# Kernel optimization log

Hardware: AMD Instinct MI355X
Metric: run time of the kernel (lower is better)

## Reference

```python
import jax, jax.numpy as jnp
import numpy as np
import math

B, T, C = 2, 2048, 2048
H, G, HS = 16, 4, 128  # n_head, n_query_groups, head_size
EPS = 1e-5
SCALE = 1.0 / math.sqrt(HS)
QKV_DIM = (H + 2 * G) * HS  # 3072, gate logits (H) appended after


def _build_rope(seq_len, n_elem, base):
    freq = base ** (np.arange(0, n_elem, 2, dtype=np.float64) / n_elem)
    inv_freq = 1.0 / freq
    idx_theta = np.outer(np.arange(seq_len, dtype=np.float64), inv_freq)
    return (jnp.asarray(np.cos(idx_theta), dtype=jnp.float32),
            jnp.asarray(np.sin(idx_theta), dtype=jnp.float32))


def setup_inputs() -> dict:
    key = jax.random.key(0)
    k1, k2, k3 = jax.random.split(key, 3)
    x = jax.random.normal(k1, (B, T, C), dtype=jnp.float32)
    # rope base per module: 0.09 * local_window ** 1.628
    base = 0.09 * (2048.0 ** 1.628)
    cos, sin = _build_rope(T, HS, base)  # [T, HS//2]
    W_attn = jax.random.normal(k2, (QKV_DIM + H, C), dtype=jnp.float32) * 0.02
    W_proj = jax.random.normal(k3, (C, H * HS), dtype=jnp.float32) * 0.02
    q_norm_w = jnp.ones((HS,), dtype=jnp.float32)
    k_norm_w = jnp.ones((HS,), dtype=jnp.float32)
    return {"x": x, "cos": cos, "sin": sin, "W_attn": W_attn,
            "q_norm_w": q_norm_w, "k_norm_w": k_norm_w, "W_proj": W_proj}


def _rms_norm(v, w):
    # per-head RMSNorm over last dim (head_size)
    ms = jnp.mean(jnp.square(v), axis=-1, keepdims=True)
    return v * jax.lax.rsqrt(ms + EPS) * w


def _apply_rope(v, cos, sin):
    # v: [B, T, N, HS]; cos/sin: [T, HS//2]; non-interleaved halves
    d2 = v.shape[-1] // 2
    x1, x2 = v[..., :d2], v[..., d2:]
    c = cos[None, :, None, :]
    s = sin[None, :, None, :]
    return jnp.concatenate([x1 * c - x2 * s, x2 * c + x1 * s], axis=-1)


def reference(x, cos, sin, W_attn, q_norm_w, k_norm_w, W_proj):
    qkv = jnp.einsum('btc,oc->bto', x, W_attn)  # [B, T, QKV_DIM+H]
    q = qkv[..., : H * HS].reshape(B, T, H, HS)
    k = qkv[..., H * HS:(H + G) * HS].reshape(B, T, G, HS)
    v = qkv[..., (H + G) * HS: QKV_DIM].reshape(B, T, G, HS)
    gate = qkv[..., QKV_DIM:]  # [B, T, H]

    q = _apply_rope(_rms_norm(q, q_norm_w), cos, sin)
    k = _apply_rope(_rms_norm(k, k_norm_w), cos, sin)

    rep = H // G
    kr = jnp.repeat(k, rep, axis=2)  # [B, T, H, HS]
    vr = jnp.repeat(v, rep, axis=2)

    scores = jnp.einsum('bthd,bshd->bhts', q, kr) * SCALE  # [B, H, T, T]
    causal = jnp.tril(jnp.ones((T, T), dtype=bool))
    scores = jnp.where(causal, scores, jnp.finfo(scores.dtype).min)
    probs = jax.nn.softmax(scores, axis=-1)
    out = jnp.einsum('bhts,bshd->bthd', probs, vr)  # [B, T, H, HS]

    out = out * jax.nn.sigmoid(gate)[..., None]  # gated attention, per-head
    y = jnp.einsum('bto,co->btc', out.reshape(B, T, H * HS), W_proj)
    return y
```

## Files before the change

kernel.cpp:

```cpp
#include <hip/hip_runtime.h>

#define T_   2048
#define BB   2
#define CC   2048
#define HH   16
#define GG   4
#define HSS  128
#define QKVD 3072
#define NQKV 3088
#define NPAD 3200
#define SCALE_ 0.08838834764831845f
#define SCALE2_ (0.08838834764831845f * 1.4426950408889634f)

typedef __attribute__((ext_vector_type(8))) short  short8;
typedef __attribute__((ext_vector_type(4))) float  f32x4;
typedef __attribute__((ext_vector_type(4))) int    v4i;
typedef __attribute__((ext_vector_type(4))) float  v4f;
typedef __attribute__((ext_vector_type(4))) unsigned short u16x4;

typedef const void __attribute__((address_space(1)))* gas1_t;
typedef void __attribute__((address_space(3)))* as3_t;

__device__ __forceinline__ void gl_lds16(const void* g, void* l) {
    __builtin_amdgcn_global_load_lds((gas1_t)g, (as3_t)l, 16, 0, 0);
}

__device__ __forceinline__ unsigned short f2bf(float f) {
    unsigned u = __float_as_uint(f);
    u += 0x7fffu + ((u >> 16) & 1u);
    return (unsigned short)(u >> 16);
}
__device__ __forceinline__ float bf2f(unsigned short h) {
    return __uint_as_float(((unsigned)h) << 16);
}

template <int CTRL>
__device__ __forceinline__ float dppmv(float x) {
    int i = __float_as_int(x);
    return __int_as_float(__builtin_amdgcn_update_dpp(i, i, CTRL, 0xF, 0xF, false));
}
__device__ __forceinline__ void red16_max(float* v) {
#pragma unroll
    for (int r = 0; r < 4; ++r) v[r] = fmaxf(v[r], dppmv<0xB1>(v[r]));
#pragma unroll
    for (int r = 0; r < 4; ++r) v[r] = fmaxf(v[r], dppmv<0x4E>(v[r]));
#pragma unroll
    for (int r = 0; r < 4; ++r) v[r] = fmaxf(v[r], dppmv<0x124>(v[r]));
#pragma unroll
    for (int r = 0; r < 4; ++r) v[r] = fmaxf(v[r], dppmv<0x128>(v[r]));
}
__device__ __forceinline__ void red16_sum(float* v) {
#pragma unroll
    for (int r = 0; r < 4; ++r) v[r] += dppmv<0xB1>(v[r]);
#pragma unroll
    for (int r = 0; r < 4; ++r) v[r] += dppmv<0x4E>(v[r]);
#pragma unroll
    for (int r = 0; r < 4; ++r) v[r] += dppmv<0x124>(v[r]);
#pragma unroll
    for (int r = 0; r < 4; ++r) v[r] += dppmv<0x128>(v[r]);
}

__global__ void k_convert3(const float* __restrict__ x, const float* __restrict__ wa,
                           const float* __restrict__ wp,
                           unsigned short* __restrict__ xb, unsigned short* __restrict__ wab,
                           unsigned short* __restrict__ wpb) {
    const int id = blockIdx.x;
    const float* src; unsigned short* dst; int base, n_src4;
    if (id < 8192)       { src = x;  dst = xb;  base = id;         n_src4 = 2097152; }
    else if (id < 14592) { src = wa; dst = wab; base = id - 8192;  n_src4 = 1581056; }
    else                 { src = wp; dst = wpb; base = id - 14592; n_src4 = 1048576; }
    int i = base * 256 + threadIdx.x;
    u16x4 o;
    if (i < n_src4) {
        v4f v = *(const v4f*)(src + (size_t)i * 4);
        o[0] = f2bf(v[0]); o[1] = f2bf(v[1]); o[2] = f2bf(v[2]); o[3] = f2bf(v[3]);
    } else {
        o[0] = 0; o[1] = 0; o[2] = 0; o[3] = 0;
    }
    *(u16x4*)(dst + (size_t)i * 4) = o;
}

template <int BM_, typename OutT>
__launch_bounds__(512, 2)
__global__ void k_gemm8(const unsigned short* __restrict__ A,
                        const unsigned short* __restrict__ Bm,
                        OutT* __restrict__ C,
                        int K, int lda, int ldb, int ldc, int nmax) {
    constexpr int MI  = BM_ / 32;
    constexpr int NPH = MI / 2;
    __shared__ unsigned short As[2][BM_ * 64];
    __shared__ unsigned short Bs[2][256 * 64];
    const int t = threadIdx.x;
    const int lane = t & 63;
    const int wid  = t >> 6;
    const int wr = wid >> 2, wc = wid & 3;
    const int bm = blockIdx.x, bn = blockIdx.y;
    const int fro = lane & 15, fk = lane >> 4;

    const int srow  = lane >> 3;
    const size_t scol = (size_t)(((lane & 7) ^ srow) * 8);

    const unsigned short* Abase = A  + (size_t)(bm * BM_) * lda;
    const unsigned short* Bbase = Bm + (size_t)(bn * 256) * ldb;

    f32x4 acc[MI][4];
#pragma unroll
    for (int i = 0; i < MI; ++i)
#pragma unroll
        for (int j = 0; j < 4; ++j) acc[i][j] = (f32x4){0.f, 0.f, 0.f, 0.f};

#pragma unroll
    for (int h = 0; h < 2; ++h)
#pragma unroll
        for (int c8 = 0; c8 < 2; ++c8) {
            const int rr = h * 128 + wid * 16 + c8 * 8;
            if (BM_ == 256 || h == 0)
                gl_lds16(Abase + (size_t)(rr + srow) * lda + scol, &As[0][rr * 64]);
            gl_lds16(Bbase + (size_t)(rr + srow) * ldb + scol, &Bs[0][rr * 64]);
        }

    int cur = 0;
    for (int kt = 0; kt < K; kt += 64) {
        asm volatile("s_waitcnt vmcnt(0)" ::: "memory");
        __builtin_amdgcn_s_barrier();
        __builtin_amdgcn_sched_barrier(0);
        const bool pf = (kt + 64 < K);
        const int nxt = cur ^ 1;
        const int kn = kt + 64;

        short8 bf_[4][2];
#pragma unroll
        for (int q = 0; q < NPH; ++q) {
            short8 af[2][2];
#pragma unroll
            for (int im = 0; im < 2; ++im)
#pragma unroll
                for (int kk = 0; kk < 2; ++kk) {
                    const int ar = wr * (BM_ / 2) + (q * 2 + im) * 16 + fro;
                    af[im][kk] = *(const short8*)&As[cur][ar * 64 + ((kk * 4 + fk) ^ (ar & 7)) * 8];
                }
            if (q == 0) {
#pragma unroll
                for (int ni = 0; ni < 4; ++ni)
#pragma unroll
                    for (int kk = 0; kk < 2; ++kk) {
                        const int br = wc * 64 + ni * 16 + fro;
                        bf_[ni][kk] = *(const short8*)&Bs[cur][br * 64 + ((kk * 4 + fk) ^ (br & 7)) * 8];
                    }
            }
            if (pf) {
                if (BM_ == 256) {
                    const int h = q & 1;
#pragma unroll
                    for (int c8 = 0; c8 < 2; ++c8) {
                        const int rr = h * 128 + wid * 16 + c8 * 8;
                        if ((q >> 1) == 0)
                            gl_lds16(Abase + (size_t)(rr + srow) * lda + kn + scol, &As[nxt][rr * 64]);
                        else
                            gl_lds16(Bbase + (size_t)(rr + srow) * ldb + kn + scol, &Bs[nxt][rr * 64]);
                    }
                } else {
                    if (q == 0) {
#pragma unroll
                        for (int c8 = 0; c8 < 2; ++c8) {
                            const int rr = wid * 16 + c8 * 8;
                            gl_lds16(Abase + (size_t)(rr + srow) * lda + kn + scol, &As[nxt][rr * 64]);
                        }
                    } else {
#pragma unroll
                        for (int h = 0; h < 2; ++h)
#pragma unroll
                            for (int c8 = 0; c8 < 2; ++c8) {
                                const int rr = h * 128 + wid * 16 + c8 * 8;
                                gl_lds16(Bbase + (size_t)(rr + srow) * ldb + kn + scol, &Bs[nxt][rr * 64]);
                            }
                    }
                }
            }
            __builtin_amdgcn_s_setprio(1);
#pragma unroll
            for (int im = 0; im < 2; ++im)
#pragma unroll
                for (int ni = 0; ni < 4; ++ni)
#pragma unroll
                    for (int kk = 0; kk < 2; ++kk)
                        acc[q * 2 + im][ni] = __builtin_amdgcn_mfma_f32_16x16x32_bf16(
                            af[im][kk], bf_[ni][kk], acc[q * 2 + im][ni], 0, 0, 0);
            __builtin_amdgcn_s_setprio(0);
            __builtin_amdgcn_s_barrier();
        }
        cur ^= 1;
    }

    const int col16 = lane & 15, rbase = (lane >> 4) * 4;
    const int gr0 = bm * BM_ + wr * (BM_ / 2);
    const int gc0 = bn * 256 + wc * 64;
#pragma unroll
    for (int mi = 0; mi < MI; ++mi)
#pragma unroll
        for (int ni = 0; ni < 4; ++ni) {
            const int gcol = gc0 + ni * 16 + col16;
            if (gcol < nmax) {
#pragma unroll
                for (int r = 0; r < 4; ++r) {
                    const int grow = gr0 + mi * 16 + rbase + r;
                    float v = acc[mi][ni][r];
                    if constexpr (sizeof(OutT) == 2)
                        C[(size_t)grow * ldc + gcol] = (OutT)f2bf(v);
                    else
                        C[(size_t)grow * ldc + gcol] = (OutT)v;
                }
            }
        }
}

__global__ void k_normtrans(unsigned short* __restrict__ qkv,
                            const float* __restrict__ cosT, const float* __restrict__ sinT,
                            const float* __restrict__ qw, const float* __restrict__ kw,
                            unsigned short* __restrict__ vt) {
    __shared__ unsigned short tile[64][65];
    const int id = blockIdx.x;
    if (id < 20480) {
        const int lane = threadIdx.x & 63;
        const int row  = id * 4 + (threadIdx.x >> 6);
        const int tok  = row / 20;
        const int hh   = row - tok * 20;
        const int tpos = tok & (T_ - 1);
        unsigned short* rp = qkv + (size_t)tok * NPAD + (hh < 16 ? hh * 128 : 2048 + (hh - 16) * 128);
        const float* w = (hh < 16) ? qw : kw;
        float e1 = bf2f(rp[lane]);
        float e2 = bf2f(rp[lane + 64]);
        float ss = e1 * e1 + e2 * e2;
#pragma unroll
        for (int m = 1; m < 64; m <<= 1) ss += __shfl_xor(ss, m);
        float inv = rsqrtf(ss * (1.0f / 128.0f) + 1e-5f);
        float n1 = e1 * inv * w[lane];
        float n2 = e2 * inv * w[lane + 64];
        float c = cosT[tpos * 64 + lane];
        float s = sinT[tpos * 64 + lane];
        rp[lane]      = f2bf(n1 * c - n2 * s);
        rp[lane + 64] = f2bf(n2 * c + n1 * s);
    } else {
        const int t2 = id - 20480;
        const int b = (t2 & 7) >> 2, g = t2 & 3;
        const int s0 = ((t2 >> 3) & 31) * 64, d0 = (t2 >> 8) * 64;
        const int tx = threadIdx.x & 63, ty0 = threadIdx.x >> 6;
        const unsigned short* src = qkv + (size_t)(b * T_ + s0) * NPAD + 2560 + g * 128 + d0;
#pragma unroll
        for (int r = 0; r < 16; ++r) {
            int ty = ty0 * 16 + r;
            tile[ty][tx] = src[(size_t)ty * NPAD + tx];
        }
        __syncthreads();
        unsigned short* dstp = vt + ((size_t)(b * GG + g) * 128 + d0) * T_ + s0;
#pragma unroll
        for (int r = 0; r < 16; ++r) {
            int ty = ty0 * 16 + r;
            dstp[(size_t)ty * T_ + tx] = tile[tx][ty];
        }
    }
}

__launch_bounds__(512, 4)
__global__ void k_attn(const unsigned short* __restrict__ qkv,
                       const unsigned short* __restrict__ vt,
                       unsigned short* __restrict__ ao) {
    __shared__ unsigned short Ks[2][64 * 128];
    __shared__ unsigned short Vs[2][128 * 64];
    __shared__ unsigned short Ps[8][16 * 64];
    const int t = threadIdx.x;
    const int lane = t & 63;
    const int wid  = t >> 6;
    const int id = blockIdx.x;
    const int bg = id & 7;
    const int hh = (id >> 3) & 3;
    const int prx = (id >> 5) & 7;
    const int pr = (id & 256) ? (15 - prx) : prx;
    const int b = bg >> 2, g = bg & 3, h = g * 4 + hh;
    const int fro = lane & 15, fk = lane >> 4;
    const int rbase = fk * 4;

    const int qt  = (wid < 4) ? pr : 31 - pr;
    const int wq  = wid & 3;
    const int q0w = qt * 64 + wq * 16;
    const int nt_own  = qt + 1;
    const int nt_loop = 32 - pr;

    const unsigned short* kg0 = qkv + (size_t)(b * T_) * NPAD + 2048 + g * 128;
    const unsigned short* vg0 = vt + (size_t)(b * GG + g) * 128 * T_;

    short8 qf[4];
    const unsigned short* qp = qkv + (size_t)(b * T_ + q0w + fro) * NPAD + h * 128 + fk * 8;
#pragma unroll
    for (int kb = 0; kb < 4; ++kb) qf[kb] = *(const short8*)(qp + kb * 32);

    float m_r[4], l_r[4];
    f32x4 o[8];
#pragma unroll
    for (int r = 0; r < 4; ++r) { m_r[r] = -1e30f; l_r[r] = 0.f; }
#pragma unroll
    for (int d = 0; d < 8; ++d) o[d] = (f32x4){0.f, 0.f, 0.f, 0.f};

    const int cp0 = wid * 2;
    int cur = 0;

#pragma unroll
    for (int p = 0; p < 2; ++p) {
        const int cp = cp0 + p;
        const int kr = cp * 4 + (lane >> 4);
        const int sK = lane & 15;
        gl_lds16(kg0 + (size_t)kr * NPAD + (size_t)((sK ^ (kr & 7)) * 8), &Ks[cur][cp * 512]);
        const int d  = cp * 8 + (lane >> 3);
        const int sV = lane & 7;
        gl_lds16(vg0 + (size_t)d * T_ + (size_t)((sV ^ (d & 7)) * 8), &Vs[cur][cp * 512]);
    }
    __syncthreads();

    for (int ti = 0; ti < nt_loop; ++ti) {
        if (ti + 1 < nt_loop) {
            const int sn = (ti + 1) * 64;
#pragma unroll
            for (int p = 0; p < 2; ++p) {
                const int cp = cp0 + p;
                const int kr = cp * 4 + (lane >> 4);
                const int sK = lane & 15;
                gl_lds16(kg0 + (size_t)(sn + kr) * NPAD + (size_t)((sK ^ (kr & 7)) * 8), &Ks[cur ^ 1][cp * 512]);
                const int d  = cp * 8 + (lane >> 3);
                const int sV = lane & 7;
                gl_lds16(vg0 + (size_t)d * T_ + sn + (size_t)((sV ^ (d & 7)) * 8), &Vs[cur ^ 1][cp * 512]);
            }
        }
        if (ti < nt_own) {
            f32x4 sc[4];
#pragma unroll
            for (int jb = 0; jb < 4; ++jb) sc[jb] = (f32x4){0.f, 0.f, 0.f, 0.f};
#pragma unroll
            for (int jb = 0; jb < 4; ++jb) {
                const int kr = jb * 16 + fro;
#pragma unroll
                for (int kb = 0; kb < 4; ++kb) {
                    short8 kf = *(const short8*)&Ks[cur][kr * 128 + 8 * ((kb * 4 + fk) ^ (kr & 7))];
                    sc[jb] = __builtin_amdgcn_mfma_f32_16x16x32_bf16(qf[kb], kf, sc[jb], 0, 0, 0);
                }
            }
            const bool domask = (ti == qt);
#pragma unroll
            for (int jb = 0; jb < 4; ++jb)
#pragma unroll
                for (int r = 0; r < 4; ++r) {
                    float v = sc[jb][r] * SCALE2_;
                    if (domask && (jb * 16 + fro) > (wq * 16 + rbase + r)) v = -1e30f;
                    sc[jb][r] = v;
                }
            float mx[4], rs[4];
#pragma unroll
            for (int r = 0; r < 4; ++r)
                mx[r] = fmaxf(fmaxf(sc[0][r], sc[1][r]), fmaxf(sc[2][r], sc[3][r]));
            red16_max(mx);
            bool grow = false;
#pragma unroll
            for (int r = 0; r < 4; ++r) grow = grow || (mx[r] > m_r[r] + 8.f);
            if (__any(grow ? 1 : 0)) {
#pragma unroll
                for (int r = 0; r < 4; ++r) {
                    float mn = fmaxf(m_r[r], mx[r]);
                    float fs = exp2f(m_r[r] - mn);
                    m_r[r] = mn;
                    l_r[r] *= fs;
#pragma unroll
                    for (int d = 0; d < 8; ++d) o[d][r] *= fs;
                }
            }
#pragma unroll
            for (int jb = 0; jb < 4; ++jb)
#pragma unroll
                for (int r = 0; r < 4; ++r) sc[jb][r] = exp2f(sc[jb][r] - m_r[r]);
#pragma unroll
            for (int r = 0; r < 4; ++r)
                rs[r] = (sc[0][r] + sc[1][r]) + (sc[2][r] + sc[3][r]);
            red16_sum(rs);
#pragma unroll
            for (int r = 0; r < 4; ++r) l_r[r] += rs[r];
            unsigned short* pw = &Ps[wid][0];
#pragma unroll
            for (int jb = 0; jb < 4; ++jb)
#pragma unroll
                for (int r = 0; r < 4; ++r) {
                    const int row = rbase + r;
                    const int slot = jb * 2 + (fro >> 3);
                    pw[row * 64 + ((slot ^ (row & 7)) * 8 + (fro & 7))] = f2bf(sc[jb][r]);
                }
            asm volatile("s_waitcnt lgkmcnt(0)" ::: "memory");
            __builtin_amdgcn_sched_barrier(0);
            short8 pa[2];
#pragma unroll
            for (int ks = 0; ks < 2; ++ks)
                pa[ks] = *(const short8*)&Ps[wid][fro * 64 + ((ks * 4 + fk) ^ (fro & 7)) * 8];
#pragma unroll
            for (int ks = 0; ks < 2; ++ks)
#pragma unroll
                for (int db = 0; db < 8; ++db) {
                    const int d = db * 16 + fro;
                    short8 vf = *(const short8*)&Vs[cur][d * 64 + 8 * ((ks * 4 + fk) ^ (d & 7))];
                    o[db] = __builtin_amdgcn_mfma_f32_16x16x32_bf16(pa[ks], vf, o[db], 0, 0, 0);
                }
        }
        __syncthreads();
        cur ^= 1;
    }
#pragma unroll
    for (int r = 0; r < 4; ++r) {
        const int qrow = q0w + rbase + r;
        float gv = bf2f(qkv[(size_t)(b * T_ + qrow) * NPAD + QKVD + h]);
        float sg = 1.f / (1.f + __expf(-gv));
        float invl = sg / l_r[r];
        unsigned short* orow = ao + (size_t)(b * T_ + qrow) * 2048 + h * 128;
#pragma unroll
        for (int db = 0; db < 8; ++db)
            orow[db * 16 + fro] = f2bf(o[db][r] * invl);
    }
}

extern "C" void kernel_launch(void* const* d_in, const int* in_sizes, int n_in,
                              void* d_out, int out_size, void* d_ws, size_t ws_size,
                              hipStream_t stream) {
    const float* x      = (const float*)d_in[0];
    const float* cosT   = (const float*)d_in[1];
    const float* sinT   = (const float*)d_in[2];
    const float* W_attn = (const float*)d_in[3];
    const float* qw     = (const float*)d_in[4];
    const float* kw     = (const float*)d_in[5];
    const float* W_proj = (const float*)d_in[6];

    char* ws = (char*)d_ws;
    const size_t OFF_XB   = 0;
    const size_t OFF_WAB  = 16777216;
    const size_t OFF_WPB  = 29884416;
    const size_t OFF_QKV  = 38273024;
    const size_t OFF_VT   = 64487424;
    const size_t OFF_AO   = 68681728;
    const size_t NEED     = 85458944;
    if (ws_size < NEED) return;

    unsigned short* xb   = (unsigned short*)(ws + OFF_XB);
    unsigned short* wab  = (unsigned short*)(ws + OFF_WAB);
    unsigned short* wpb  = (unsigned short*)(ws + OFF_WPB);
    unsigned short* qkvb = (unsigned short*)(ws + OFF_QKV);
    unsigned short* vtb  = (unsigned short*)(ws + OFF_VT);
    unsigned short* aob  = (unsigned short*)(ws + OFF_AO);

    k_convert3<<<18688, 256, 0, stream>>>(x, W_attn, W_proj, xb, wab, wpb);
    k_gemm8<256, unsigned short><<<dim3(16, 13), 512, 0, stream>>>(xb, wab, qkvb, 2048, 2048, 2048, NPAD, NPAD);
    k_normtrans<<<20992, 256, 0, stream>>>(qkvb, cosT, sinT, qw, kw, vtb);
    k_attn<<<512, 512, 0, stream>>>(qkvb, vtb, aob);
    k_gemm8<128, float><<<dim3(32, 8), 512, 0, stream>>>(aob, wpb, (float*)d_out, 2048, 2048, 2048, 2048, 2048);
}
```

Before: 212.0 us.

## Single-buffer K/V tiles for higher occupancy and fold softmax scale into Q

Drops the double-buffered K/V LDS tiles for a single buffer loaded synchronously each iteration, which halves LDS use so launch bounds can ask for 6 waves per SIMD instead of 4. The softmax scale (with log2e) moves into the Q norm/rope kernel so the attention inner loop no longer multiplies every score. The P-to-bf16 conversion switches to a cheaper round-half-up. In exchange, global-to-LDS loads no longer overlap compute inside a block, so the design relies on the extra co-resident blocks to hide that latency, and Q is rounded to bf16 after scaling.

Result: slower. 374.2 us (+76.5%).

```diff
diff --git a/kernel.cpp b/kernel.cpp
--- a/kernel.cpp
+++ b/kernel.cpp
@@ -29,6 +29,9 @@
     unsigned u = __float_as_uint(f);
     u += 0x7fffu + ((u >> 16) & 1u);
     return (unsigned short)(u >> 16);
+}
+__device__ __forceinline__ unsigned short f2bf_fast(float f) {
+    return (unsigned short)((__float_as_uint(f) + 0x8000u) >> 16);
 }
 __device__ __forceinline__ float bf2f(unsigned short h) {
     return __uint_as_float(((unsigned)h) << 16);
@@ -228,6 +231,7 @@
         const int tpos = tok & (T_ - 1);
         unsigned short* rp = qkv + (size_t)tok * NPAD + (hh < 16 ? hh * 128 : 2048 + (hh - 16) * 128);
         const float* w = (hh < 16) ? qw : kw;
+        const float sc_ = (hh < 16) ? SCALE2_ : 1.0f;
         float e1 = bf2f(rp[lane]);
         float e2 = bf2f(rp[lane + 64]);
         float ss = e1 * e1 + e2 * e2;
@@ -238,8 +242,8 @@
         float n2 = e2 * inv * w[lane + 64];
         float c = cosT[tpos * 64 + lane];
         float s = sinT[tpos * 64 + lane];
-        rp[lane]      = f2bf(n1 * c - n2 * s);
-        rp[lane + 64] = f2bf(n2 * c + n1 * s);
+        rp[lane]      = f2bf((n1 * c - n2 * s) * sc_);
+        rp[lane + 64] = f2bf((n2 * c + n1 * s) * sc_);
     } else {
         const int t2 = id - 20480;
         const int b = (t2 & 7) >> 2, g = t2 & 3;
@@ -261,12 +265,12 @@
     }
 }
 
-__launch_bounds__(512, 4)
+__launch_bounds__(512, 6)
 __global__ void k_attn(const unsigned short* __restrict__ qkv,
                        const unsigned short* __restrict__ vt,
                        unsigned short* __restrict__ ao) {
-    __shared__ unsigned short Ks[2][64 * 128];
-    __shared__ unsigned short Vs[2][128 * 64];
+    __shared__ unsigned short Ks[64 * 128];
+    __shared__ unsigned short Vs[128 * 64];
     __shared__ unsigned short Ps[8][16 * 64];
     const int t = threadIdx.x;
     const int lane = t & 63;
@@ -302,34 +306,22 @@
     for (int d = 0; d < 8; ++d) o[d] = (f32x4){0.f, 0.f, 0.f, 0.f};
 
     const int cp0 = wid * 2;
-    int cur = 0;
-
-#pragma unroll
-    for (int p = 0; p < 2; ++p) {
-        const int cp = cp0 + p;
-        const int kr = cp * 4 + (lane >> 4);
-        const int sK = lane & 15;
-        gl_lds16(kg0 + (size_t)kr * NPAD + (size_t)((sK ^ (kr & 7)) * 8), &Ks[cur][cp * 512]);
-        const int d  = cp * 8 + (lane >> 3);
-        const int sV = lane & 7;
-        gl_lds16(vg0 + (size_t)d * T_ + (size_t)((sV ^ (d & 7)) * 8), &Vs[cur][cp * 512]);
-    }
-    __syncthreads();
 
     for (int ti = 0; ti < nt_loop; ++ti) {
-        if (ti + 1 < nt_loop) {
-            const int sn = (ti + 1) * 64;
-#pragma unroll
-            for (int p = 0; p < 2; ++p) {
-                const int cp = cp0 + p;
-                const int kr = cp * 4 + (lane >> 4);
-                const int sK = lane & 15;
-                gl_lds16(kg0 + (size_t)(sn + kr) * NPAD + (size_t)((sK ^ (kr & 7)) * 8), &Ks[cur ^ 1][cp * 512]);
-                const int d  = cp * 8 + (lane >> 3);
-                const int sV = lane & 7;
-                gl_lds16(vg0 + (size_t)d * T_ + sn + (size_t)((sV ^ (d & 7)) * 8), &Vs[cur ^ 1][cp * 512]);
-            }
-        }
+        const int s0 = ti * 64;
+        __syncthreads();
+#pragma unroll
+        for (int p = 0; p < 2; ++p) {
+            const int cp = cp0 + p;
+            const int kr = cp * 4 + (lane >> 4);
+            const int sK = lane & 15;
+            gl_lds16(kg0 + (size_t)(s0 + kr) * NPAD + (size_t)((sK ^ (kr & 7)) * 8), &Ks[cp * 512]);
+            const int d  = cp * 8 + (lane >> 3);
+            const int sV = lane & 7;
+            gl_lds16(vg0 + (size_t)d * T_ + s0 + (size_t)((sV ^ (d & 7)) * 8), &Vs[cp * 512]);
+        }
+        __syncthreads();
+
         if (ti < nt_own) {
             f32x4 sc[4];
 #pragma unroll
@@ -339,19 +331,17 @@
                 const int kr = jb * 16 + fro;
 #pragma unroll
                 for (int kb = 0; kb < 4; ++kb) {
-                    short8 kf = *(const short8*)&Ks[cur][kr * 128 + 8 * ((kb * 4 + fk) ^ (kr & 7))];
+                    short8 kf = *(const short8*)&Ks[kr * 128 + 8 * ((kb * 4 + fk) ^ (kr & 7))];
                     sc[jb] = __builtin_amdgcn_mfma_f32_16x16x32_bf16(qf[kb], kf, sc[jb], 0, 0, 0);
                 }
             }
-            const bool domask = (ti == qt);
-#pragma unroll
-            for (int jb = 0; jb < 4; ++jb)
-#pragma unroll
-                for (int r = 0; r < 4; ++r) {
-                    float v = sc[jb][r] * SCALE2_;
-                    if (domask && (jb * 16 + fro) > (wq * 16 + rbase + r)) v = -1e30f;
-                    sc[jb][r] = v;
-                }
+            if (ti == qt) {
+#pragma unroll
+                for (int jb = 0; jb < 4; ++jb)
+#pragma unroll
+                    for (int r = 0; r < 4; ++r)
+                        if ((jb * 16 + fro) > (wq * 16 + rbase + r)) sc[jb][r] = -1e30f;
+            }
             float mx[4], rs[4];
 #pragma unroll
             for (int r = 0; r < 4; ++r)
@@ -388,7 +378,7 @@
                 for (int r = 0; r < 4; ++r) {
                     const int row = rbase + r;
                     const int slot = jb * 2 + (fro >> 3);
-                    pw[row * 64 + ((slot ^ (row & 7)) * 8 + (fro & 7))] = f2bf(sc[jb][r]);
+                    pw[row * 64 + ((slot ^ (row & 7)) * 8 + (fro & 7))] = f2bf_fast(sc[jb][r]);
                 }
             asm volatile("s_waitcnt lgkmcnt(0)" ::: "memory");
             __builtin_amdgcn_sched_barrier(0);
@@ -401,12 +391,10 @@
 #pragma unroll
                 for (int db = 0; db < 8; ++db) {
                     const int d = db * 16 + fro;
-                    short8 vf = *(const short8*)&Vs[cur][d * 64 + 8 * ((ks * 4 + fk) ^ (d & 7))];
+                    short8 vf = *(const short8*)&Vs[d * 64 + 8 * ((ks * 4 + fk) ^ (d & 7))];
                     o[db] = __builtin_amdgcn_mfma_f32_16x16x32_bf16(pa[ks], vf, o[db], 0, 0, 0);
                 }
         }
-        __syncthreads();
-        cur ^= 1;
     }
 #pragma unroll
     for (int r = 0; r < 4; ++r) {
```
